# Optimization experiments

Hardware: AMD Instinct MI355X
Metric: run time of the kernel (lower is better)

Reference implementation:

```python
import jax, jax.numpy as jnp
import numpy as np

N = 25000      # nodes
E = 400000     # edges (before self-loops)
F_IN = 128     # num_node_features
HID = 16       # hidden_channels
HEADS = 12     # GAT heads
OUT = 32       # output_channels


def setup_inputs() -> dict:
    key = jax.random.key(0)
    ks = jax.random.split(key, 16)
    def glorot(k, shape):
        fan_in = shape[0]
        return jax.random.normal(k, shape, jnp.float32) / np.sqrt(fan_in)
    return {
        "x": jax.random.normal(ks[0], (N, 1, F_IN), jnp.float32),
        "edge_index": jax.random.randint(ks[1], (2, E), 0, N, jnp.int64),
        # GCNConv 1
        "W1": glorot(ks[2], (F_IN, HID)),
        "b1": jnp.zeros((HID,), jnp.float32),
        # GATConv (heads=12, concat)
        "Wg": glorot(ks[3], (HID, HEADS * HID)),
        "att_src": jax.random.normal(ks[4], (HEADS, HID), jnp.float32) * 0.1,
        "att_dst": jax.random.normal(ks[5], (HEADS, HID), jnp.float32) * 0.1,
        "bg": jnp.zeros((HEADS * HID,), jnp.float32),
        # GCNConv 2 and 3
        "W2": glorot(ks[6], (HEADS * HID, HID)),
        "b2": jnp.zeros((HID,), jnp.float32),
        "W3": glorot(ks[7], (HID, HID)),
        "b3": jnp.zeros((HID,), jnp.float32),
        # final Linear
        "Wlin": glorot(ks[8], (HID, OUT)),
        "blin": jnp.zeros((OUT,), jnp.float32),
    }


def _add_self_loops(edge_index, n):
    loop = jnp.arange(n, dtype=edge_index.dtype)
    src = jnp.concatenate([edge_index[0], loop])
    dst = jnp.concatenate([edge_index[1], loop])
    return src, dst


def _gcn_conv(x, W, b, src, dst, n):
    # PyG GCNConv: symmetric normalization with self-loops (already in src/dst)
    h = x @ W                                            # [N, C]
    deg = jax.ops.segment_sum(jnp.ones_like(dst, jnp.float32), dst, n)
    dinv = jnp.where(deg > 0, jax.lax.rsqrt(deg), 0.0)   # deg^-0.5
    norm = dinv[src] * dinv[dst]                         # [E']
    out = jax.ops.segment_sum(h[src] * norm[:, None], dst, n)
    return out + b


def _gat_conv(x, Wg, att_src, att_dst, bg, src, dst, n):
    # PyG GATConv, concat=True, negative_slope=0.2, self-loops in src/dst
    h = (x @ Wg).reshape(n, HEADS, HID)                  # [N, H, C]
    a_s = jnp.sum(h * att_src, axis=-1)                  # [N, H]
    a_d = jnp.sum(h * att_dst, axis=-1)                  # [N, H]
    e = a_s[src] + a_d[dst]                              # [E', H]
    e = jnp.where(e > 0, e, 0.2 * e)                     # leaky_relu
    m = jax.ops.segment_max(e, dst, n)                   # stable softmax per dst
    ex = jnp.exp(e - m[dst])
    denom = jax.ops.segment_sum(ex, dst, n)
    alpha = ex / denom[dst]                              # [E', H]
    out = jax.ops.segment_sum(alpha[:, :, None] * h[src], dst, n)  # [N, H, C]
    return out.reshape(n, HEADS * HID) + bg


def reference(x, edge_index, W1, b1, Wg, att_src, att_dst, bg, W2, b2, W3, b3, Wlin, blin):
    n = x.shape[0]
    src, dst = _add_self_loops(edge_index, n)
    xs = x.squeeze(1)                                    # [N, F]
    x1 = jax.nn.relu(_gcn_conv(xs, W1, b1, src, dst, n))
    # dropout p=0.5 is identity in eval mode
    x2 = jax.nn.elu(_gat_conv(x1, Wg, att_src, att_dst, bg, src, dst, n))
    x3 = jax.nn.relu(_gcn_conv(x2, W2, b2, src, dst, n))
    x4 = jax.nn.relu(_gcn_conv(x3, W3, b3, src, dst, n)) + x3
    x4 = jnp.mean(x4, axis=0, keepdims=True)             # [1, HID]
    return x4 @ Wlin + blin                              # [1, OUT]
```

## Files before the change

### kernel.cpp

```cpp
#include <hip/hip_runtime.h>

#define F_IN 128
#define HID 16
#define HEADS 12
#define HF (HEADS*HID)
#define OUT_C 32

__global__ void k_detect(const int* __restrict__ ei, int E, int* __restrict__ flag) {
    __shared__ int sacc[256];
    int t = threadIdx.x;
    long long half = (long long)E;
    int acc = 0;
    #pragma unroll
    for (int i = 0; i < 8; i++) {
        long long k = ((long long)(t + i * 256) * half) / 2048;
        acc |= ei[2 * k + 1];
    }
    sacc[t] = acc;
    __syncthreads();
    for (int off = 128; off >= 1; off >>= 1) {
        if (t < off) sacc[t] |= sacc[t + off];
        __syncthreads();
    }
    if (t == 0) flag[1] = sacc[0];
}

__global__ void k_convert(const void* __restrict__ ei, int E, const int* __restrict__ flag,
                          int* __restrict__ src32, int* __restrict__ dst32,
                          int* __restrict__ count) {
    int e = blockIdx.x * blockDim.x + threadIdx.x;
    if (e >= E) return;
    int s, d;
    if (flag[1] == 0) {
        const long long* p = (const long long*)ei;
        s = (int)p[e];
        d = (int)p[(size_t)E + e];
    } else {
        const int* p = (const int*)ei;
        s = p[e];
        d = p[(size_t)E + e];
    }
    src32[e] = s;
    dst32[e] = d;
    atomicAdd(&count[d], 1);
}


__global__ void k_scan(const int* __restrict__ count, int* __restrict__ rowstart,
                       float* __restrict__ dinv, int n) {
    __shared__ int part[1024];
    int t = threadIdx.x;
    int chunk = (n + 1023) >> 10;
    int beg = t * chunk;
    int end = beg + chunk; if (end > n) end = n;
    int s = 0;
    for (int i = beg; i < end; i++) s += count[i];
    part[t] = s;
    __syncthreads();
    for (int off = 1; off < 1024; off <<= 1) {
        int v = (t >= off) ? part[t - off] : 0;
        __syncthreads();
        part[t] += v;
        __syncthreads();
    }
    int run = (t == 0) ? 0 : part[t - 1];
    for (int i = beg; i < end; i++) {
        rowstart[i] = run;
        int c = count[i];
        run += c;
        dinv[i] = rsqrtf((float)(c + 1));
    }
    if (t == 1023) rowstart[n] = run;
}

__global__ void k_fill(const int* __restrict__ srcA, const int* __restrict__ dstA, int E,
                       const int* __restrict__ rowstart, int* __restrict__ cursor,
                       int* __restrict__ csr) {
    int e = blockIdx.x * blockDim.x + threadIdx.x;
    if (e < E) {
        int d = dstA[e];
        int p = atomicAdd(&cursor[d], 1);
        csr[rowstart[d] + p] = srcA[e];
    }
}


__global__ void k_gemm1(const float* __restrict__ x, const float* __restrict__ W,
                        float* __restrict__ h, int n) {
    __shared__ float sW[F_IN * HID];
    __shared__ float sX[16][F_IN + 1];
    int t = threadIdx.x;
    for (int i = t; i < F_IN * HID; i += 256) sW[i] = W[i];
    int node0 = blockIdx.x * 16;
    for (int i = t; i < 16 * F_IN; i += 256) {
        int r = i >> 7, c = i & 127;
        int node = node0 + r;
        sX[r][c] = (node < n) ? x[node * F_IN + c] : 0.f;
    }
    __syncthreads();
    int ln = t >> 4, c = t & 15;
    float acc = 0.f;
    #pragma unroll 8
    for (int k = 0; k < F_IN; k++) acc += sX[ln][k] * sW[k * HID + c];
    int node = node0 + ln;
    if (node < n) h[node * HID + c] = acc;
}

__global__ void k_gemm_gat(const float* __restrict__ x1, const float* __restrict__ Wg,
                           const float* __restrict__ att_s, const float* __restrict__ att_d,
                           float* __restrict__ hg, float* __restrict__ a_s,
                           float* __restrict__ a_d, int n) {
    int c = threadIdx.x;
    int lane = c & 63;
    int hh = c >> 4, ci = c & 15;
    float ats = att_s[c];
    float atd = att_d[c];
    float wcol[HID];
    #pragma unroll
    for (int k = 0; k < HID; k++) wcol[k] = Wg[k * HF + c];
    for (int node = blockIdx.x; node < n; node += gridDim.x) {
        float xv = x1[node * HID + (lane & 15)];
        float acc = 0.f;
        #pragma unroll
        for (int k = 0; k < HID; k++) acc += __shfl(xv, k) * wcol[k];
        hg[(size_t)node * HF + c] = acc;
        float vs = acc * ats, vd = acc * atd;
        #pragma unroll
        for (int msk = 8; msk >= 1; msk >>= 1) {
            vs += __shfl_xor(vs, msk);
            vd += __shfl_xor(vd, msk);
        }
        if (ci == 0) {
            a_s[node * HEADS + hh] = vs;
            a_d[node * HEADS + hh] = vd;
        }
    }
}

__global__ void k_gemm2(const float* __restrict__ x2, const float* __restrict__ W,
                        float* __restrict__ h, int n) {
    __shared__ float sW[HF * HID];
    __shared__ float sX[16][HF + 1];
    int t = threadIdx.x;
    for (int i = t; i < HF * HID; i += 256) sW[i] = W[i];
    int node0 = blockIdx.x * 16;
    for (int i = t; i < 16 * HF; i += 256) {
        int r = i / HF, c = i % HF;
        int node = node0 + r;
        sX[r][c] = (node < n) ? x2[(size_t)node * HF + c] : 0.f;
    }
    __syncthreads();
    int ln = t >> 4, c = t & 15;
    float acc = 0.f;
    #pragma unroll 8
    for (int k = 0; k < HF; k++) acc += sX[ln][k] * sW[k * HID + c];
    int node = node0 + ln;
    if (node < n) h[node * HID + c] = acc;
}

__global__ void k_gemm3(const float* __restrict__ x3, const float* __restrict__ W,
                        float* __restrict__ h, int n) {
    __shared__ float sW[HID * HID];
    __shared__ float sX[16][HID + 1];
    int t = threadIdx.x;
    sW[t] = W[t];
    int node0 = blockIdx.x * 16;
    int r = t >> 4, cc = t & 15;
    int nd = node0 + r;
    sX[r][cc] = (nd < n) ? x3[nd * HID + cc] : 0.f;
    __syncthreads();
    float acc = 0.f;
    #pragma unroll
    for (int k = 0; k < HID; k++) acc += sX[r][k] * sW[k * HID + cc];
    if (nd < n) h[nd * HID + cc] = acc;
}


__global__ void k_gcn_agg(const float* __restrict__ h, const int* __restrict__ rowstart,
                          const int* __restrict__ csr, const float* __restrict__ dinv,
                          const float* __restrict__ bias, const float* __restrict__ resid,
                          float* __restrict__ out, int n) {
    int node = (blockIdx.x * blockDim.x + threadIdx.x) >> 6;
    int lane = threadIdx.x & 63;
    if (node >= n) return;
    int c = lane & 15, jj = lane >> 4;
    float dn = dinv[node];
    int base = rowstart[node], deg = rowstart[node + 1] - base;
    float acc = (jj == 0) ? h[node * HID + c] * dn : 0.f;
    int j = jj;
    for (; j + 4 < deg; j += 8) {
        int s0 = csr[base + j], s1 = csr[base + j + 4];
        float d0 = dinv[s0], d1 = dinv[s1];
        float h0 = h[s0 * HID + c], h1 = h[s1 * HID + c];
        acc += h0 * d0 + h1 * d1;
    }
    if (j < deg) {
        int s0 = csr[base + j];
        acc += h[s0 * HID + c] * dinv[s0];
    }
    acc += __shfl_xor(acc, 16);
    acc += __shfl_xor(acc, 32);
    if (lane < 16) {
        float v = fmaxf(acc * dn + bias[c], 0.f);
        if (resid) v += resid[node * HID + c];
        out[node * HID + c] = v;
    }
}

__global__ void k_gat_agg(const float* __restrict__ hg, const float* __restrict__ a_s,
                          const float* __restrict__ a_d, const int* __restrict__ rowstart,
                          const int* __restrict__ csr, const float* __restrict__ bg,
                          float* __restrict__ x2, int n) {
    int node = (blockIdx.x * blockDim.x + threadIdx.x) >> 6;
    int lane = threadIdx.x & 63;
    if (node >= n) return;
    int base = rowstart[node], deg = rowstart[node + 1] - base;

    int hA = lane % 12;
    int hh0 = lane >> 4;
    int hh1 = (lane + 64) >> 4;
    int hh2 = (lane + 128) >> 4;

    float adA = a_d[node * HEADS + hA];
    float e0 = a_s[node * HEADS + hA] + adA;
    e0 = (e0 > 0.f) ? e0 : 0.2f * e0;
    float m = e0, s = 1.f;
    float acc0 = hg[(size_t)node * HF + lane];
    float acc1 = hg[(size_t)node * HF + lane + 64];
    float acc2 = hg[(size_t)node * HF + lane + 128];

#define GAT_EDGE(AS, G0, G1, G2)                                      \
    {                                                                 \
        float e = (AS) + adA;                                         \
        e = (e > 0.f) ? e : 0.2f * e;                                 \
        float d = e - m;                                              \
        float p = __expf(d);                                          \
        if (__any(d > 8.f)) {                       \
            bool big = d > 8.f;                                       \
            float rp = big ? __expf(-d) : 1.f;                        \
            float pe = big ? 1.f : p;                                 \
            s = s * rp + pe;                                          \
            if (big) m = e;                                           \
            acc0 = acc0 * __shfl(rp, hh0) + __shfl(pe, hh0) * (G0);   \
            acc1 = acc1 * __shfl(rp, hh1) + __shfl(pe, hh1) * (G1);   \
            acc2 = acc2 * __shfl(rp, hh2) + __shfl(pe, hh2) * (G2);   \
        } else {                                                      \
            s += p;                                                   \
            acc0 += __shfl(p, hh0) * (G0);                            \
            acc1 += __shfl(p, hh1) * (G1);                            \
            acc2 += __shfl(p, hh2) * (G2);                            \
        }                                                             \
    }

    int j = 0;
    for (; j + 2 <= deg; j += 2) {
        int s0 = csr[base + j], s1 = csr[base + j + 1];
        float as0 = a_s[s0 * HEADS + hA];
        float as1 = a_s[s1 * HEADS + hA];
        float g00 = hg[(size_t)s0 * HF + lane];
        float g01 = hg[(size_t)s0 * HF + lane + 64];
        float g02 = hg[(size_t)s0 * HF + lane + 128];
        float g10 = hg[(size_t)s1 * HF + lane];
        float g11 = hg[(size_t)s1 * HF + lane + 64];
        float g12 = hg[(size_t)s1 * HF + lane + 128];
        GAT_EDGE(as0, g00, g01, g02)
        GAT_EDGE(as1, g10, g11, g12)
    }
    if (j < deg) {
        int s0 = csr[base + j];
        float as0 = a_s[s0 * HEADS + hA];
        float g00 = hg[(size_t)s0 * HF + lane];
        float g01 = hg[(size_t)s0 * HF + lane + 64];
        float g02 = hg[(size_t)s0 * HF + lane + 128];
        GAT_EDGE(as0, g00, g01, g02)
    }
#undef GAT_EDGE

    float is = 1.f / s;
    float i0 = __shfl(is, hh0), i1 = __shfl(is, hh1), i2 = __shfl(is, hh2);
    float v0 = acc0 * i0 + bg[lane];
    float v1 = acc1 * i1 + bg[lane + 64];
    float v2 = acc2 * i2 + bg[lane + 128];
    v0 = (v0 > 0.f) ? v0 : (__expf(v0) - 1.f);
    v1 = (v1 > 0.f) ? v1 : (__expf(v1) - 1.f);
    v2 = (v2 > 0.f) ? v2 : (__expf(v2) - 1.f);
    x2[(size_t)node * HF + lane]       = v0;
    x2[(size_t)node * HF + lane + 64]  = v1;
    x2[(size_t)node * HF + lane + 128] = v2;
}


__global__ void k_mean(const float* __restrict__ x4, float* __restrict__ red, int n) {
    __shared__ float sd[16][17];
    int t = threadIdx.x;
    int ln = t >> 4, c = t & 15;
    float acc = 0.f;
    for (int node = blockIdx.x * 16 + ln; node < n; node += gridDim.x * 16)
        acc += x4[node * HID + c];
    sd[ln][c] = acc;
    __syncthreads();
    for (int off = 8; off >= 1; off >>= 1) {
        if (ln < off) sd[ln][c] += sd[ln + off][c];
        __syncthreads();
    }
    if (ln == 0) atomicAdd(&red[c], sd[0][c]);
}

__global__ void k_final(const float* __restrict__ red, const float* __restrict__ Wlin,
                        const float* __restrict__ blin, float* __restrict__ out, float invN) {
    int o = threadIdx.x;
    if (o >= OUT_C) return;
    float acc = blin[o];
    #pragma unroll
    for (int c = 0; c < HID; c++) acc += (red[c] * invN) * Wlin[c * OUT_C + o];
    out[o] = acc;
}


extern "C" void kernel_launch(void* const* d_in, const int* in_sizes, int n_in,
                              void* d_out, int out_size, void* d_ws, size_t ws_size,
                              hipStream_t stream) {
    const float* x     = (const float*)d_in[0];
    const void*  ei    = d_in[1];
    const float* W1    = (const float*)d_in[2];
    const float* b1    = (const float*)d_in[3];
    const float* Wg    = (const float*)d_in[4];
    const float* att_s = (const float*)d_in[5];
    const float* att_d = (const float*)d_in[6];
    const float* bg    = (const float*)d_in[7];
    const float* W2    = (const float*)d_in[8];
    const float* b2    = (const float*)d_in[9];
    const float* W3    = (const float*)d_in[10];
    const float* b3    = (const float*)d_in[11];
    const float* Wlin  = (const float*)d_in[12];
    const float* blin  = (const float*)d_in[13];
    float* out = (float*)d_out;

    int N = in_sizes[0] / F_IN;
    int E = in_sizes[1] / 2;

    char* w = (char*)d_ws;
    size_t off = 0;
    auto alloc = [&](size_t bytes) -> void* {
        void* p = w + off;
        off += (bytes + 255) & ~(size_t)255;
        return p;
    };
    int*   flag     = (int*)alloc(256);
    int*   count    = (int*)alloc((size_t)N * 4);
    int*   cursor   = (int*)alloc((size_t)N * 4);
    float* red      = (float*)alloc(64);
    size_t zbytes   = (size_t)((char*)red + 256 - (char*)count);
    int*   src32    = (int*)alloc((size_t)E * 4);
    int*   dst32    = (int*)alloc((size_t)E * 4);
    int*   rowstart = (int*)alloc((size_t)(N + 1) * 4);
    int*   csr      = (int*)alloc((size_t)E * 4);
    float* dinv     = (float*)alloc((size_t)N * 4);
    float* h1       = (float*)alloc((size_t)N * HID * 4);
    float* x1       = (float*)alloc((size_t)N * HID * 4);
    float* hg       = (float*)alloc((size_t)N * HF * 4);
    float* a_s      = (float*)alloc((size_t)N * HEADS * 4);
    float* a_d      = (float*)alloc((size_t)N * HEADS * 4);
    float* x2       = (float*)alloc((size_t)N * HF * 4);
    float* h2       = (float*)alloc((size_t)N * HID * 4);
    float* x3       = (float*)alloc((size_t)N * HID * 4);
    float* h3       = (float*)alloc((size_t)N * HID * 4);
    float* x4       = (float*)alloc((size_t)N * HID * 4);
    if (off > ws_size) return;

    hipMemsetAsync(count, 0, zbytes, stream);

    int eb = (E + 255) / 256;
    int nb16 = (N + 15) / 16;
    int nbw  = (N + 3) / 4;

    k_detect<<<1, 256, 0, stream>>>((const int*)ei, E, flag);
    k_convert<<<eb, 256, 0, stream>>>(ei, E, flag, src32, dst32, count);
    k_scan<<<1, 1024, 0, stream>>>(count, rowstart, dinv, N);
    k_fill<<<eb, 256, 0, stream>>>(src32, dst32, E, rowstart, cursor, csr);

    k_gemm1<<<nb16, 256, 0, stream>>>(x, W1, h1, N);
    k_gcn_agg<<<nbw, 256, 0, stream>>>(h1, rowstart, csr, dinv, b1, nullptr, x1, N);

    k_gemm_gat<<<2048, 192, 0, stream>>>(x1, Wg, att_s, att_d, hg, a_s, a_d, N);
    k_gat_agg<<<nbw, 256, 0, stream>>>(hg, a_s, a_d, rowstart, csr, bg, x2, N);

    k_gemm2<<<nb16, 256, 0, stream>>>(x2, W2, h2, N);
    k_gcn_agg<<<nbw, 256, 0, stream>>>(h2, rowstart, csr, dinv, b2, nullptr, x3, N);

    k_gemm3<<<nb16, 256, 0, stream>>>(x3, W3, h3, N);
    k_gcn_agg<<<nbw, 256, 0, stream>>>(h3, rowstart, csr, dinv, b3, x3, x4, N);

    k_mean<<<128, 256, 0, stream>>>(x4, red, N);
    k_final<<<1, 64, 0, stream>>>(red, Wlin, blin, out, 1.0f / (float)N);
}
```

Baseline: 336.1 us.

## Fuse W2 and W3 GEMMs into preceding aggregation kernels and preload edge indices

Fuses the 192-to-16 projection with W2 into the GAT aggregation epilogue using per-lane partial products and a butterfly shuffle reduction, so the N×192 x2 tensor is never written or read back. Likewise fuses the 16×16 W3 projection into the second GCN aggregation. The GAT loop now loads up to 64 neighbour indices cooperatively into lanes and broadcasts them by shuffle, unrolled by four to put more gathers in flight. This removes two kernel launches and a large intermediate write and read, at the cost of 16 registers of partials plus 96 shuffles per node, which may add register pressure.

```diff
diff --git a/kernel.cpp b/kernel.cpp
--- a/kernel.cpp
+++ b/kernel.cpp
@@ -137,44 +137,6 @@
     }
 }
 
-__global__ void k_gemm2(const float* __restrict__ x2, const float* __restrict__ W,
-                        float* __restrict__ h, int n) {
-    __shared__ float sW[HF * HID];
-    __shared__ float sX[16][HF + 1];
-    int t = threadIdx.x;
-    for (int i = t; i < HF * HID; i += 256) sW[i] = W[i];
-    int node0 = blockIdx.x * 16;
-    for (int i = t; i < 16 * HF; i += 256) {
-        int r = i / HF, c = i % HF;
-        int node = node0 + r;
-        sX[r][c] = (node < n) ? x2[(size_t)node * HF + c] : 0.f;
-    }
-    __syncthreads();
-    int ln = t >> 4, c = t & 15;
-    float acc = 0.f;
-    #pragma unroll 8
-    for (int k = 0; k < HF; k++) acc += sX[ln][k] * sW[k * HID + c];
-    int node = node0 + ln;
-    if (node < n) h[node * HID + c] = acc;
-}
-
-__global__ void k_gemm3(const float* __restrict__ x3, const float* __restrict__ W,
-                        float* __restrict__ h, int n) {
-    __shared__ float sW[HID * HID];
-    __shared__ float sX[16][HID + 1];
-    int t = threadIdx.x;
-    sW[t] = W[t];
-    int node0 = blockIdx.x * 16;
-    int r = t >> 4, cc = t & 15;
-    int nd = node0 + r;
-    sX[r][cc] = (nd < n) ? x3[nd * HID + cc] : 0.f;
-    __syncthreads();
-    float acc = 0.f;
-    #pragma unroll
-    for (int k = 0; k < HID; k++) acc += sX[r][k] * sW[k * HID + cc];
-    if (nd < n) h[nd * HID + cc] = acc;
-}
-
 
 __global__ void k_gcn_agg(const float* __restrict__ h, const int* __restrict__ rowstart,
                           const int* __restrict__ csr, const float* __restrict__ dinv,
@@ -207,14 +169,50 @@
     }
 }
 
+__global__ void k_gcn_agg_f3(const float* __restrict__ h, const int* __restrict__ rowstart,
+                             const int* __restrict__ csr, const float* __restrict__ dinv,
+                             const float* __restrict__ bias, const float* __restrict__ W3,
+                             float* __restrict__ x3o, float* __restrict__ h3o, int n) {
+    int node = (blockIdx.x * blockDim.x + threadIdx.x) >> 6;
+    int lane = threadIdx.x & 63;
+    if (node >= n) return;
+    int c = lane & 15, jj = lane >> 4;
+    float dn = dinv[node];
+    int base = rowstart[node], deg = rowstart[node + 1] - base;
+    float acc = (jj == 0) ? h[node * HID + c] * dn : 0.f;
+    int j = jj;
+    for (; j + 4 < deg; j += 8) {
+        int s0 = csr[base + j], s1 = csr[base + j + 4];
+        float d0 = dinv[s0], d1 = dinv[s1];
+        float h0 = h[s0 * HID + c], h1 = h[s1 * HID + c];
+        acc += h0 * d0 + h1 * d1;
+    }
+    if (j < deg) {
+        int s0 = csr[base + j];
+        acc += h[s0 * HID + c] * dinv[s0];
+    }
+    acc += __shfl_xor(acc, 16);
+    acc += __shfl_xor(acc, 32);
+    float v = fmaxf(acc * dn + bias[c], 0.f);
+    if (lane < 16) x3o[node * HID + c] = v;
+    int gbase = lane & 48;
+    float hacc = 0.f;
+    #pragma unroll
+    for (int cc = 0; cc < 16; cc++)
+        hacc += __shfl(v, gbase | cc) * W3[cc * HID + c];
+    if (lane < 16) h3o[node * HID + c] = hacc;
+}
+
 __global__ void k_gat_agg(const float* __restrict__ hg, const float* __restrict__ a_s,
                           const float* __restrict__ a_d, const int* __restrict__ rowstart,
                           const int* __restrict__ csr, const float* __restrict__ bg,
-                          float* __restrict__ x2, int n) {
+                          const float* __restrict__ W2, float* __restrict__ h2, int n) {
     int node = (blockIdx.x * blockDim.x + threadIdx.x) >> 6;
     int lane = threadIdx.x & 63;
     if (node >= n) return;
     int base = rowstart[node], deg = rowstart[node + 1] - base;
+    int dcap = deg < 64 ? deg : 64;
+    int eidx = (lane < dcap) ? csr[base + lane] : 0;
 
     int hA = lane % 12;
     int hh0 = lane >> 4;
@@ -253,26 +251,31 @@
     }
 
     int j = 0;
-    for (; j + 2 <= deg; j += 2) {
-        int s0 = csr[base + j], s1 = csr[base + j + 1];
-        float as0 = a_s[s0 * HEADS + hA];
-        float as1 = a_s[s1 * HEADS + hA];
-        float g00 = hg[(size_t)s0 * HF + lane];
-        float g01 = hg[(size_t)s0 * HF + lane + 64];
-        float g02 = hg[(size_t)s0 * HF + lane + 128];
-        float g10 = hg[(size_t)s1 * HF + lane];
-        float g11 = hg[(size_t)s1 * HF + lane + 64];
-        float g12 = hg[(size_t)s1 * HF + lane + 128];
-        GAT_EDGE(as0, g00, g01, g02)
-        GAT_EDGE(as1, g10, g11, g12)
-    }
-    if (j < deg) {
+    for (; j + 4 <= dcap; j += 4) {
+        int s0 = __shfl(eidx, j),     s1 = __shfl(eidx, j + 1);
+        int s2 = __shfl(eidx, j + 2), s3 = __shfl(eidx, j + 3);
+        float A0 = a_s[s0 * HEADS + hA], A1 = a_s[s1 * HEADS + hA];
+        float A2 = a_s[s2 * HEADS + hA], A3 = a_s[s3 * HEADS + hA];
+        float g00 = hg[(size_t)s0 * HF + lane], g01 = hg[(size_t)s0 * HF + lane + 64], g02 = hg[(size_t)s0 * HF + lane + 128];
+        float g10 = hg[(size_t)s1 * HF + lane], g11 = hg[(size_t)s1 * HF + lane + 64], g12 = hg[(size_t)s1 * HF + lane + 128];
+        float g20 = hg[(size_t)s2 * HF + lane], g21 = hg[(size_t)s2 * HF + lane + 64], g22 = hg[(size_t)s2 * HF + lane + 128];
+        float g30 = hg[(size_t)s3 * HF + lane], g31 = hg[(size_t)s3 * HF + lane + 64], g32 = hg[(size_t)s3 * HF + lane + 128];
+        GAT_EDGE(A0, g00, g01, g02)
+        GAT_EDGE(A1, g10, g11, g12)
+        GAT_EDGE(A2, g20, g21, g22)
+        GAT_EDGE(A3, g30, g31, g32)
+    }
+    for (; j < dcap; j++) {
+        int s0 = __shfl(eidx, j);
+        float A0 = a_s[s0 * HEADS + hA];
+        float g00 = hg[(size_t)s0 * HF + lane], g01 = hg[(size_t)s0 * HF + lane + 64], g02 = hg[(size_t)s0 * HF + lane + 128];
+        GAT_EDGE(A0, g00, g01, g02)
+    }
+    for (; j < deg; j++) {
         int s0 = csr[base + j];
-        float as0 = a_s[s0 * HEADS + hA];
-        float g00 = hg[(size_t)s0 * HF + lane];
-        float g01 = hg[(size_t)s0 * HF + lane + 64];
-        float g02 = hg[(size_t)s0 * HF + lane + 128];
-        GAT_EDGE(as0, g00, g01, g02)
+        float A0 = a_s[s0 * HEADS + hA];
+        float g00 = hg[(size_t)s0 * HF + lane], g01 = hg[(size_t)s0 * HF + lane + 64], g02 = hg[(size_t)s0 * HF + lane + 128];
+        GAT_EDGE(A0, g00, g01, g02)
     }
 #undef GAT_EDGE
 
@@ -284,9 +287,25 @@
     v0 = (v0 > 0.f) ? v0 : (__expf(v0) - 1.f);
     v1 = (v1 > 0.f) ? v1 : (__expf(v1) - 1.f);
     v2 = (v2 > 0.f) ? v2 : (__expf(v2) - 1.f);
-    x2[(size_t)node * HF + lane]       = v0;
-    x2[(size_t)node * HF + lane + 64]  = v1;
-    x2[(size_t)node * HF + lane + 128] = v2;
+
+    float p[16];
+    const float4* W2v = (const float4*)W2;
+    #pragma unroll
+    for (int q = 0; q < 4; q++) {
+        float4 w0 = W2v[lane * 4 + q];
+        float4 w1 = W2v[(lane + 64) * 4 + q];
+        float4 w2 = W2v[(lane + 128) * 4 + q];
+        p[q * 4 + 0] = v0 * w0.x + v1 * w1.x + v2 * w2.x;
+        p[q * 4 + 1] = v0 * w0.y + v1 * w1.y + v2 * w2.y;
+        p[q * 4 + 2] = v0 * w0.z + v1 * w1.z + v2 * w2.z;
+        p[q * 4 + 3] = v0 * w0.w + v1 * w1.w + v2 * w2.w;
+    }
+    #pragma unroll
+    for (int mask = 1; mask <= 32; mask <<= 1) {
+        #pragma unroll
+        for (int cq = 0; cq < 16; cq++) p[cq] += __shfl_xor(p[cq], mask);
+    }
+    if (lane < 16) h2[node * HID + lane] = p[lane];
 }
 
 
@@ -361,7 +380,6 @@
     float* hg       = (float*)alloc((size_t)N * HF * 4);
     float* a_s      = (float*)alloc((size_t)N * HEADS * 4);
     float* a_d      = (float*)alloc((size_t)N * HEADS * 4);
-    float* x2       = (float*)alloc((size_t)N * HF * 4);
     float* h2       = (float*)alloc((size_t)N * HID * 4);
     float* x3       = (float*)alloc((size_t)N * HID * 4);
     float* h3       = (float*)alloc((size_t)N * HID * 4);
@@ -383,12 +401,9 @@
     k_gcn_agg<<<nbw, 256, 0, stream>>>(h1, rowstart, csr, dinv, b1, nullptr, x1, N);
 
     k_gemm_gat<<<2048, 192, 0, stream>>>(x1, Wg, att_s, att_d, hg, a_s, a_d, N);
-    k_gat_agg<<<nbw, 256, 0, stream>>>(hg, a_s, a_d, rowstart, csr, bg, x2, N);
-
-    k_gemm2<<<nb16, 256, 0, stream>>>(x2, W2, h2, N);
-    k_gcn_agg<<<nbw, 256, 0, stream>>>(h2, rowstart, csr, dinv, b2, nullptr, x3, N);
-
-    k_gemm3<<<nb16, 256, 0, stream>>>(x3, W3, h3, N);
+    k_gat_agg<<<nbw, 256, 0, stream>>>(hg, a_s, a_d, rowstart, csr, bg, W2, h2, N);
+
+    k_gcn_agg_f3<<<nbw, 256, 0, stream>>>(h2, rowstart, csr, dinv, b2, W3, x3, h3, N);
     k_gcn_agg<<<nbw, 256, 0, stream>>>(h3, rowstart, csr, dinv, b3, x3, x4, N);
 
     k_mean<<<128, 256, 0, stream>>>(x4, red, N);
```

Measured after the change: 316.3 us. -5.9%, faster.
